# Optimization experiments

Measured on AMD Instinct MI355X. Metric: run time of the kernel, lower is better.

Reference implementation:

```python
import jax, jax.numpy as jnp
import numpy as np

N_NODES = 20000
N_EDGES = 320000
F_IN = 256
N_HID = 128
MID = 800


def _glorot(key, shape):
    fan_in, fan_out = shape
    s = jnp.sqrt(6.0 / (fan_in + fan_out))
    return jax.random.uniform(key, shape, jnp.float32, -s, s)


def setup_inputs() -> dict:
    key = jax.random.key(0)
    ks = jax.random.split(key, 8)
    x = jax.random.normal(ks[0], (N_NODES, F_IN), jnp.float32)
    src = jax.random.randint(ks[1], (N_EDGES,), 0, N_NODES)
    dst = jax.random.randint(ks[2], (N_EDGES,), 0, N_NODES)
    return {
        "x": x, "src": src, "dst": dst,
        "W1": _glorot(ks[3], (F_IN, MID)), "b1": jnp.zeros((MID,), jnp.float32),
        "W2": _glorot(ks[4], (MID, N_HID)), "b2": jnp.zeros((N_HID,), jnp.float32),
        "W3": _glorot(ks[5], (N_HID, MID)), "b3": jnp.zeros((MID,), jnp.float32),
        "W4": _glorot(ks[6], (MID, F_IN)), "b4": jnp.zeros((F_IN,), jnp.float32),
    }


def _deg_rsqrt(idx, n):
    # clamp(min=1) as in DGL GraphConv norm='both'
    deg = jax.ops.segment_sum(jnp.ones(idx.shape[0], jnp.float32), idx, num_segments=n)
    return jax.lax.rsqrt(jnp.maximum(deg, 1.0))


def _graph_conv(x, W, b, src, dst, n, act):
    # DGL GraphConv, norm='both': out = D_in^{-1/2} A D_out^{-1/2} X W + b
    ns = _deg_rsqrt(src, n)  # src-side (out-degree) norm
    nd = _deg_rsqrt(dst, n)  # dst-side (in-degree) norm
    in_f, out_f = W.shape
    if in_f > out_f:
        # multiply by W first (smaller aggregation width), as DGL does
        h = (x @ W) * ns[:, None]
        h = jax.ops.segment_sum(h[src], dst, num_segments=n)
    else:
        h = x * ns[:, None]
        h = jax.ops.segment_sum(h[src], dst, num_segments=n) @ W
    h = h * nd[:, None] + b
    return act(h) if act is not None else h


def reference(x, src, dst, W1, b1, W2, b2, W3, b3, W4, b4):
    n = x.shape[0]
    h = _graph_conv(x, W1, b1, src, dst, n, jax.nn.relu)   # [N, 800]
    h = _graph_conv(h, W2, b2, src, dst, n, None)          # [N, 128]
    encoded = jax.nn.sigmoid(h)
    h = _graph_conv(h, W3, b3, src, dst, n, jax.nn.relu)   # [N, 800]
    h = _graph_conv(h, W4, b4, src, dst, n, None)          # [N, 256]
    decoded = jax.nn.sigmoid(h)
    return (encoded, decoded)
```

## Files before the change

### kernel.cpp

```cpp
#include <hip/hip_runtime.h>
#include <math.h>

constexpr int NN = 20000;
constexpr int NE = 320000;
constexpr int MROWS = 20224;
constexpr int SB = 79;

typedef __bf16 bf16x8 __attribute__((ext_vector_type(8)));
typedef float f32x4 __attribute__((ext_vector_type(4)));

__device__ __forceinline__ unsigned short f2bf(float f) {
  unsigned int u = __float_as_uint(f);
  unsigned int r = (u + 0x7FFFu + ((u >> 16) & 1u)) >> 16;
  return (unsigned short)r;
}

__global__ __launch_bounds__(256) void zero_kernel(int4* __restrict__ p, int n4) {
  int i = blockIdx.x * 256 + threadIdx.x;
  if (i < n4) p[i] = make_int4(0, 0, 0, 0);
}

__global__ void deg_count_kernel(const int* __restrict__ src, const int* __restrict__ dst,
                                 int* __restrict__ degs, int* __restrict__ degd, int nE) {
  int e = blockIdx.x * blockDim.x + threadIdx.x;
  if (e < nE) {
    atomicAdd(degs + src[e], 1);
    atomicAdd(degd + dst[e], 1);
  }
}

__global__ __launch_bounds__(256) void pscan_norm_kernel(
    const int* __restrict__ degs, const int* __restrict__ degd,
    int* __restrict__ pscan, int* __restrict__ bsum,
    float* __restrict__ ns, float* __restrict__ nd, int n) {
  __shared__ int s[256];
  int t = threadIdx.x;
  int idx = blockIdx.x * 256 + t;
  int val = 0;
  if (idx < n) {
    int dd = degd[idx];
    val = dd;
    ns[idx] = rsqrtf(fmaxf((float)degs[idx], 1.0f));
    nd[idx] = rsqrtf(fmaxf((float)dd, 1.0f));
  }
  s[t] = val;
  __syncthreads();
#pragma unroll
  for (int off = 1; off < 256; off <<= 1) {
    int v = (t >= off) ? s[t - off] : 0;
    __syncthreads();
    s[t] += v;
    __syncthreads();
  }
  if (idx < n) pscan[idx] = s[t] - val;
  if (t == 255) bsum[blockIdx.x] = s[255];
}

__global__ __launch_bounds__(256) void rowptr_fix_kernel(
    const int* __restrict__ pscan, const int* __restrict__ bsum,
    int* __restrict__ rowptr, int n) {
  __shared__ int s[128];
  int t = threadIdx.x;
  if (t < 128) s[t] = (t < SB) ? bsum[t] : 0;
  __syncthreads();
#pragma unroll
  for (int off = 1; off < 128; off <<= 1) {
    int v = (t < 128 && t >= off) ? s[t - off] : 0;
    __syncthreads();
    if (t < 128) s[t] += v;
    __syncthreads();
  }
  int idx = blockIdx.x * 256 + t;
  int boff = (blockIdx.x == 0) ? 0 : s[blockIdx.x - 1];
  if (idx < n) rowptr[idx] = pscan[idx] + boff;
  if (idx == 0) rowptr[n] = NE;
}

__global__ void csr_fill_kernel(const int* __restrict__ src, const int* __restrict__ dst,
                                const int* __restrict__ rowptr, int* __restrict__ cursor,
                                int* __restrict__ col, int nE) {
  int e = blockIdx.x * blockDim.x + threadIdx.x;
  if (e < nE) {
    int d = dst[e];
    int p = atomicAdd(cursor + d, 1);
    col[rowptr[d] + p] = src[e];
  }
}

__global__ __launch_bounds__(256) void wt_convert_all_kernel(
    const float* __restrict__ W1, const float* __restrict__ W2,
    const float* __restrict__ W3, const float* __restrict__ W4,
    unsigned short* __restrict__ W1t, unsigned short* __restrict__ W2t,
    unsigned short* __restrict__ W3t, unsigned short* __restrict__ W4t) {
  int n = blockIdx.y;
  int k = blockIdx.x * 256 + threadIdx.x;
  const float* W; unsigned short* Wt; int K, N, Kpad;
  if (n < 832)       { W = W1; Wt = W1t; K = 256; N = 800; Kpad = 256; }
  else if (n < 960)  { n -= 832;  W = W2; Wt = W2t; K = 800; N = 128; Kpad = 832; }
  else if (n < 1792) { n -= 960;  W = W3; Wt = W3t; K = 128; N = 800; Kpad = 128; }
  else               { n -= 1792; W = W4; Wt = W4t; K = 800; N = 256; Kpad = 832; }
  if (k >= Kpad) return;
  float v = (n < N && k < K) ? W[(size_t)k * N + n] : 0.f;
  Wt[(size_t)n * Kpad + k] = f2bf(v);
}

__global__ __launch_bounds__(256) void scale_cvt_kernel(
    const float* __restrict__ x, const float* __restrict__ ns,
    unsigned short* __restrict__ xb) {
  int t = blockIdx.x * 256 + threadIdx.x;
  if (t >= NN * 32) return;
  int node = t >> 5;
  float sc = ns[node];
  float4 v1 = reinterpret_cast<const float4*>(x)[t * 2];
  float4 v2 = reinterpret_cast<const float4*>(x)[t * 2 + 1];
  uint4 o;
  o.x = f2bf(v1.x * sc) | ((unsigned)f2bf(v1.y * sc) << 16);
  o.y = f2bf(v1.z * sc) | ((unsigned)f2bf(v1.w * sc) << 16);
  o.z = f2bf(v2.x * sc) | ((unsigned)f2bf(v2.y * sc) << 16);
  o.w = f2bf(v2.z * sc) | ((unsigned)f2bf(v2.w * sc) << 16);
  reinterpret_cast<uint4*>(xb)[t] = o;
}

template <int F, int EPI>
__global__ __launch_bounds__(256) void gatherb_kernel(
    const unsigned short* __restrict__ in, const int* __restrict__ rowptr,
    const int* __restrict__ col, const float* __restrict__ sDst,
    const float* __restrict__ bias, const float* __restrict__ snext,
    unsigned short* __restrict__ out, float* __restrict__ out2, int n) {
  constexpr int LPN = F / 8;
  constexpr int NPB = 256 / LPN;
  const int tid = threadIdx.x;
  const int node = blockIdx.x * NPB + tid / LPN;
  const int j = tid % LPN;
  if (node >= n) return;
  const int e0 = rowptr[node], e1 = rowptr[node + 1];
  float a[8] = {0.f, 0.f, 0.f, 0.f, 0.f, 0.f, 0.f, 0.f};
  int e = e0;
  for (; e + 1 < e1; e += 2) {
    int c0 = col[e], c1 = col[e + 1];
    uint4 u0 = *reinterpret_cast<const uint4*>(in + (size_t)c0 * F + j * 8);
    uint4 u1 = *reinterpret_cast<const uint4*>(in + (size_t)c1 * F + j * 8);
    a[0] += __uint_as_float(u0.x << 16);
    a[1] += __uint_as_float(u0.x & 0xffff0000u);
    a[2] += __uint_as_float(u0.y << 16);
    a[3] += __uint_as_float(u0.y & 0xffff0000u);
    a[4] += __uint_as_float(u0.z << 16);
    a[5] += __uint_as_float(u0.z & 0xffff0000u);
    a[6] += __uint_as_float(u0.w << 16);
    a[7] += __uint_as_float(u0.w & 0xffff0000u);
    a[0] += __uint_as_float(u1.x << 16);
    a[1] += __uint_as_float(u1.x & 0xffff0000u);
    a[2] += __uint_as_float(u1.y << 16);
    a[3] += __uint_as_float(u1.y & 0xffff0000u);
    a[4] += __uint_as_float(u1.z << 16);
    a[5] += __uint_as_float(u1.z & 0xffff0000u);
    a[6] += __uint_as_float(u1.w << 16);
    a[7] += __uint_as_float(u1.w & 0xffff0000u);
  }
  if (e < e1) {
    int c = col[e];
    uint4 u = *reinterpret_cast<const uint4*>(in + (size_t)c * F + j * 8);
    a[0] += __uint_as_float(u.x << 16);
    a[1] += __uint_as_float(u.x & 0xffff0000u);
    a[2] += __uint_as_float(u.y << 16);
    a[3] += __uint_as_float(u.y & 0xffff0000u);
    a[4] += __uint_as_float(u.z << 16);
    a[5] += __uint_as_float(u.z & 0xffff0000u);
    a[6] += __uint_as_float(u.w << 16);
    a[7] += __uint_as_float(u.w & 0xffff0000u);
  }
  if (EPI == 0) {
    uint4 o;
    o.x = f2bf(a[0]) | ((unsigned)f2bf(a[1]) << 16);
    o.y = f2bf(a[2]) | ((unsigned)f2bf(a[3]) << 16);
    o.z = f2bf(a[4]) | ((unsigned)f2bf(a[5]) << 16);
    o.w = f2bf(a[6]) | ((unsigned)f2bf(a[7]) << 16);
    *reinterpret_cast<uint4*>(out + (size_t)node * F + j * 8) = o;
    return;
  }
  const float sd = sDst[node];
  float v[8];
#pragma unroll
  for (int k = 0; k < 8; ++k) v[k] = a[k] * sd + bias[j * 8 + k];
  if (EPI == 1) {
    float sn = snext[node];
    uint4 o;
    o.x = f2bf(v[0] * sn) | ((unsigned)f2bf(v[1] * sn) << 16);
    o.y = f2bf(v[2] * sn) | ((unsigned)f2bf(v[3] * sn) << 16);
    o.z = f2bf(v[4] * sn) | ((unsigned)f2bf(v[5] * sn) << 16);
    o.w = f2bf(v[6] * sn) | ((unsigned)f2bf(v[7] * sn) << 16);
    *reinterpret_cast<uint4*>(out + (size_t)node * F + j * 8) = o;
  }
  float4 s1, s2;
  s1.x = 1.0f / (1.0f + expf(-v[0]));
  s1.y = 1.0f / (1.0f + expf(-v[1]));
  s1.z = 1.0f / (1.0f + expf(-v[2]));
  s1.w = 1.0f / (1.0f + expf(-v[3]));
  s2.x = 1.0f / (1.0f + expf(-v[4]));
  s2.y = 1.0f / (1.0f + expf(-v[5]));
  s2.z = 1.0f / (1.0f + expf(-v[6]));
  s2.w = 1.0f / (1.0f + expf(-v[7]));
  *reinterpret_cast<float4*>(out2 + (size_t)node * F + j * 8) = s1;
  *reinterpret_cast<float4*>(out2 + (size_t)node * F + j * 8 + 4) = s2;
}

template <int KT1, int NOUT>
__global__ __launch_bounds__(256) void gemm9v2_kernel(
    const unsigned short* __restrict__ A,
    const unsigned short* __restrict__ Wa,
    const unsigned short* __restrict__ Wb,
    unsigned short* __restrict__ Out,
    int M, const float* __restrict__ nd, const float* __restrict__ ns,
    const float* __restrict__ ba) {
  constexpr int K1 = KT1 * 32;
  constexpr int N2 = NOUT * 16;
  constexpr int ROWB1 = K1 * 2;
  constexpr int CPR1 = K1 / 8;
  constexpr int W1B = 64 * ROWB1;
  constexpr int W2B = N2 * 128;
  constexpr int HST = 144;
  __shared__ __align__(16) char lds[W1B + W2B + 4 * 16 * HST];

  const int tid = threadIdx.x;
  const int l = tid & 63, w = tid >> 6;
  const int lrow = l & 15, k16 = l >> 4;
  const int m0 = blockIdx.x * 64 + w * 16;
  char* const w1p = lds;
  char* const w2s = lds + W1B;
  char* const h1t = lds + W1B + W2B + w * 16 * HST;

  auto stage = [&](int nt) {
#pragma unroll
    for (int i = 0; i < 64 * CPR1 / 256; ++i) {
      int c = i * 256 + tid;
      int row = c / CPR1, lch = c % CPR1;
      int gch = (lch & ~7) | ((lch & 7) ^ (row & 7));
      const unsigned short* gp = Wa + (size_t)(nt * 64 + row) * K1 + gch * 8;
      __builtin_amdgcn_global_load_lds(
          (const __attribute__((address_space(1))) void*)gp,
          (__attribute__((address_space(3))) void*)(w1p + (i * 256 + w * 64) * 16), 16, 0, 0);
    }
#pragma unroll
    for (int i = 0; i < N2 * 8 / 256; ++i) {
      int c = i * 256 + tid;
      int row = c >> 3, lch = c & 7;
      int gch = lch ^ (row & 7);
      const unsigned short* gp = Wb + (size_t)row * 832 + nt * 64 + gch * 8;
      __builtin_amdgcn_global_load_lds(
          (const __attribute__((address_space(1))) void*)gp,
          (__attribute__((address_space(3))) void*)(w2s + (i * 256 + w * 64) * 16), 16, 0, 0);
    }
  };

  bf16x8 af[KT1];
#pragma unroll
  for (int t = 0; t < KT1; ++t)
    af[t] = *reinterpret_cast<const bf16x8*>(
        A + (size_t)(m0 + lrow) * K1 + t * 32 + k16 * 8);

  stage(0);
  __syncthreads();

  f32x4 acc2[NOUT] = {};
  for (int nt = 0; nt < 13; ++nt) {
    f32x4 acc1[4] = {};
#pragma unroll
    for (int t = 0; t < KT1; ++t) {
      bf16x8 bf[4];
#pragma unroll
      for (int ni = 0; ni < 4; ++ni) {
        int row = ni * 16 + lrow;
        int ch = t * 4 + k16;
        int sc = (ch & ~7) | ((ch & 7) ^ (row & 7));
        bf[ni] = *reinterpret_cast<const bf16x8*>(w1p + row * ROWB1 + sc * 16);
      }
#pragma unroll
      for (int ni = 0; ni < 4; ++ni)
        acc1[ni] = __builtin_amdgcn_mfma_f32_16x16x32_bf16(af[t], bf[ni], acc1[ni], 0, 0, 0);
    }

#pragma unroll
    for (int q = 0; q < 4; ++q) {
      int rl = k16 * 4 + q;
      float rs = nd[m0 + rl];
#pragma unroll
      for (int ni = 0; ni < 4; ++ni) {
        int colc = ni * 16 + lrow;
        int jg = nt * 64 + colc;
        float bb = (jg < 800) ? ba[jg] : 0.f;
        float v = fmaxf(acc1[ni][q] * rs + bb, 0.f);
        *(unsigned short*)(h1t + rl * HST + (colc >> 3) * 16 + (colc & 7) * 2) = f2bf(v);
      }
    }

#pragma unroll
    for (int ks = 0; ks < 2; ++ks) {
      bf16x8 a2 = *reinterpret_cast<const bf16x8*>(h1t + lrow * HST + (ks * 4 + k16) * 16);
#pragma unroll
      for (int ni = 0; ni < NOUT; ++ni) {
        int rc = ni * 16 + lrow;
        int sc = (ks * 4 + k16) ^ (rc & 7);
        bf16x8 b2v = *reinterpret_cast<const bf16x8*>(w2s + rc * 128 + sc * 16);
        acc2[ni] = __builtin_amdgcn_mfma_f32_16x16x32_bf16(a2, b2v, acc2[ni], 0, 0, 0);
      }
    }
    __syncthreads();
    if (nt + 1 < 13) {
      stage(nt + 1);
      __syncthreads();
    }
  }

#pragma unroll
  for (int q = 0; q < 4; ++q) {
    int r = m0 + k16 * 4 + q;
    if (r >= M) continue;
    float sn = ns[r];
#pragma unroll
    for (int ni = 0; ni < NOUT; ++ni) {
      int c = ni * 16 + lrow;
      Out[(size_t)r * N2 + c] = f2bf(acc2[ni][q] * sn);
    }
  }
}

extern "C" void kernel_launch(void* const* d_in, const int* in_sizes, int n_in,
                              void* d_out, int out_size, void* d_ws, size_t ws_size,
                              hipStream_t stream) {
  const float* x  = (const float*)d_in[0];
  const int* src  = (const int*)d_in[1];
  const int* dst  = (const int*)d_in[2];
  const float* W1 = (const float*)d_in[3];
  const float* b1 = (const float*)d_in[4];
  const float* W2 = (const float*)d_in[5];
  const float* b2 = (const float*)d_in[6];
  const float* W3 = (const float*)d_in[7];
  const float* b3 = (const float*)d_in[8];
  const float* W4 = (const float*)d_in[9];
  const float* b4 = (const float*)d_in[10];

  float* out_enc = (float*)d_out;
  float* out_dec = out_enc + (size_t)NN * 128;

  float* ns = (float*)d_ws;
  float* nd = ns + NN;
  unsigned short* xb  = (unsigned short*)(nd + NN);
  unsigned short* T2b = xb + (size_t)NN * 256;
  unsigned short* h2  = T2b + (size_t)NN * 128;
  unsigned short* A1  = h2 + (size_t)NN * 128;
  unsigned short* A3  = A1 + (size_t)MROWS * 256;
  unsigned short* G4  = A3 + (size_t)MROWS * 128;
  unsigned short* W1t = G4 + (size_t)NN * 256;
  unsigned short* W2t = W1t + 832 * 256;
  unsigned short* W3t = W2t + 128 * 832;
  unsigned short* W4t = W3t + 832 * 128;
  int* degs   = (int*)(W4t + 256 * 832);
  int* degd   = degs + NN;
  int* cursor = degd + NN;
  int* rowptr = cursor + NN;
  int* col    = rowptr + NN + 1;
  int* pscan  = col + NE;
  int* bsum   = pscan + NN;

  zero_kernel<<<(3 * NN / 4 + 255) / 256, 256, 0, stream>>>((int4*)degs, 3 * NN / 4);
  deg_count_kernel<<<(NE + 255) / 256, 256, 0, stream>>>(src, dst, degs, degd, NE);
  pscan_norm_kernel<<<SB, 256, 0, stream>>>(degs, degd, pscan, bsum, ns, nd, NN);
  rowptr_fix_kernel<<<SB, 256, 0, stream>>>(pscan, bsum, rowptr, NN);
  csr_fill_kernel<<<(NE + 255) / 256, 256, 0, stream>>>(src, dst, rowptr, cursor, col, NE);

  wt_convert_all_kernel<<<dim3(4, 2048), 256, 0, stream>>>(
      W1, W2, W3, W4, W1t, W2t, W3t, W4t);

  scale_cvt_kernel<<<(NN * 32 + 255) / 256, 256, 0, stream>>>(x, ns, xb);
  gatherb_kernel<256, 0><<<(NN + 7) / 8, 256, 0, stream>>>(
      xb, rowptr, col, nullptr, nullptr, nullptr, A1, nullptr, NN);
  gemm9v2_kernel<8, 8><<<314, 256, 0, stream>>>(A1, W1t, W2t, T2b, NN, nd, ns, b1);

  gatherb_kernel<128, 1><<<(NN + 15) / 16, 256, 0, stream>>>(
      T2b, rowptr, col, nd, b2, ns, h2, out_enc, NN);

  gatherb_kernel<128, 0><<<(NN + 15) / 16, 256, 0, stream>>>(
      h2, rowptr, col, nullptr, nullptr, nullptr, A3, nullptr, NN);
  gemm9v2_kernel<4, 16><<<314, 256, 0, stream>>>(A3, W3t, W4t, G4, NN, nd, ns, b3);

  gatherb_kernel<256, 2><<<(NN + 7) / 8, 256, 0, stream>>>(
      G4, rowptr, col, nd, b4, nullptr, nullptr, out_dec, NN);
}
```

Before: 245.0 us.

## Split fused GEMM N-tiles across wave halves and read weights directly from global

The fused two-layer GEMM kernel no longer stages weight tiles into LDS with per-tile barriers. Instead each wave loads weight fragments straight from global memory, relying on L2/cache reuse. Each block now covers 32 rows, with the 13 middle-dimension tiles split between two wave pairs (7 and 6 tiles). The partial second-layer accumulators are reduced through LDS, and the launch grid doubles to 628 blocks. This removes the per-iteration __syncthreads and the LDS staging, and adds parallelism. The cost is more global/L2 weight traffic, uncoalesced-ish fragment loads, and a slightly unbalanced split.

```diff
diff --git a/kernel.cpp b/kernel.cpp
--- a/kernel.cpp
+++ b/kernel.cpp
@@ -205,7 +205,7 @@
 }
 
 template <int KT1, int NOUT>
-__global__ __launch_bounds__(256) void gemm9v2_kernel(
+__global__ __launch_bounds__(256) void gemm10_kernel(
     const unsigned short* __restrict__ A,
     const unsigned short* __restrict__ Wa,
     const unsigned short* __restrict__ Wb,
@@ -214,43 +214,19 @@
     const float* __restrict__ ba) {
   constexpr int K1 = KT1 * 32;
   constexpr int N2 = NOUT * 16;
-  constexpr int ROWB1 = K1 * 2;
-  constexpr int CPR1 = K1 / 8;
-  constexpr int W1B = 64 * ROWB1;
-  constexpr int W2B = N2 * 128;
   constexpr int HST = 144;
-  __shared__ __align__(16) char lds[W1B + W2B + 4 * 16 * HST];
+  constexpr int CST = N2 * 4 + 16;
+  constexpr int HTB = 4 * 16 * HST;
+  constexpr int CMB = 32 * CST;
+  constexpr int LDSB = (CMB > HTB ? CMB : HTB);
+  __shared__ __align__(16) char lds[LDSB];
 
   const int tid = threadIdx.x;
   const int l = tid & 63, w = tid >> 6;
+  const int wr = w & 1, half = w >> 1;
   const int lrow = l & 15, k16 = l >> 4;
-  const int m0 = blockIdx.x * 64 + w * 16;
-  char* const w1p = lds;
-  char* const w2s = lds + W1B;
-  char* const h1t = lds + W1B + W2B + w * 16 * HST;
-
-  auto stage = [&](int nt) {
-#pragma unroll
-    for (int i = 0; i < 64 * CPR1 / 256; ++i) {
-      int c = i * 256 + tid;
-      int row = c / CPR1, lch = c % CPR1;
-      int gch = (lch & ~7) | ((lch & 7) ^ (row & 7));
-      const unsigned short* gp = Wa + (size_t)(nt * 64 + row) * K1 + gch * 8;
-      __builtin_amdgcn_global_load_lds(
-          (const __attribute__((address_space(1))) void*)gp,
-          (__attribute__((address_space(3))) void*)(w1p + (i * 256 + w * 64) * 16), 16, 0, 0);
-    }
-#pragma unroll
-    for (int i = 0; i < N2 * 8 / 256; ++i) {
-      int c = i * 256 + tid;
-      int row = c >> 3, lch = c & 7;
-      int gch = lch ^ (row & 7);
-      const unsigned short* gp = Wb + (size_t)row * 832 + nt * 64 + gch * 8;
-      __builtin_amdgcn_global_load_lds(
-          (const __attribute__((address_space(1))) void*)gp,
-          (__attribute__((address_space(3))) void*)(w2s + (i * 256 + w * 64) * 16), 16, 0, 0);
-    }
-  };
+  const int m0 = blockIdx.x * 32 + wr * 16;
+  char* const h1t = lds + w * 16 * HST;
 
   bf16x8 af[KT1];
 #pragma unroll
@@ -258,22 +234,17 @@
     af[t] = *reinterpret_cast<const bf16x8*>(
         A + (size_t)(m0 + lrow) * K1 + t * 32 + k16 * 8);
 
-  stage(0);
-  __syncthreads();
-
   f32x4 acc2[NOUT] = {};
-  for (int nt = 0; nt < 13; ++nt) {
+  const int ntEnd = half ? 13 : 7;
+  for (int nt = half ? 7 : 0; nt < ntEnd; ++nt) {
     f32x4 acc1[4] = {};
 #pragma unroll
     for (int t = 0; t < KT1; ++t) {
       bf16x8 bf[4];
 #pragma unroll
-      for (int ni = 0; ni < 4; ++ni) {
-        int row = ni * 16 + lrow;
-        int ch = t * 4 + k16;
-        int sc = (ch & ~7) | ((ch & 7) ^ (row & 7));
-        bf[ni] = *reinterpret_cast<const bf16x8*>(w1p + row * ROWB1 + sc * 16);
-      }
+      for (int ni = 0; ni < 4; ++ni)
+        bf[ni] = *reinterpret_cast<const bf16x8*>(
+            Wa + (size_t)(nt * 64 + ni * 16 + lrow) * K1 + t * 32 + k16 * 8);
 #pragma unroll
       for (int ni = 0; ni < 4; ++ni)
         acc1[ni] = __builtin_amdgcn_mfma_f32_16x16x32_bf16(af[t], bf[ni], acc1[ni], 0, 0, 0);
@@ -298,28 +269,39 @@
       bf16x8 a2 = *reinterpret_cast<const bf16x8*>(h1t + lrow * HST + (ks * 4 + k16) * 16);
 #pragma unroll
       for (int ni = 0; ni < NOUT; ++ni) {
-        int rc = ni * 16 + lrow;
-        int sc = (ks * 4 + k16) ^ (rc & 7);
-        bf16x8 b2v = *reinterpret_cast<const bf16x8*>(w2s + rc * 128 + sc * 16);
+        bf16x8 b2v = *reinterpret_cast<const bf16x8*>(
+            Wb + (size_t)(ni * 16 + lrow) * 832 + nt * 64 + (ks * 4 + k16) * 8);
         acc2[ni] = __builtin_amdgcn_mfma_f32_16x16x32_bf16(a2, b2v, acc2[ni], 0, 0, 0);
       }
     }
-    __syncthreads();
-    if (nt + 1 < 13) {
-      stage(nt + 1);
-      __syncthreads();
-    }
-  }
-
-#pragma unroll
-  for (int q = 0; q < 4; ++q) {
-    int r = m0 + k16 * 4 + q;
-    if (r >= M) continue;
-    float sn = ns[r];
-#pragma unroll
-    for (int ni = 0; ni < NOUT; ++ni) {
-      int c = ni * 16 + lrow;
-      Out[(size_t)r * N2 + c] = f2bf(acc2[ni][q] * sn);
+  }
+
+  __syncthreads();
+  if (half) {
+#pragma unroll
+    for (int q = 0; q < 4; ++q) {
+      int rl = wr * 16 + k16 * 4 + q;
+#pragma unroll
+      for (int ni = 0; ni < NOUT; ++ni) {
+        int c = ni * 16 + lrow;
+        *(float*)(lds + rl * CST + c * 4) = acc2[ni][q];
+      }
+    }
+  }
+  __syncthreads();
+  if (!half) {
+#pragma unroll
+    for (int q = 0; q < 4; ++q) {
+      int r = m0 + k16 * 4 + q;
+      if (r >= M) continue;
+      int rl = wr * 16 + k16 * 4 + q;
+      float sn = ns[r];
+#pragma unroll
+      for (int ni = 0; ni < NOUT; ++ni) {
+        int c = ni * 16 + lrow;
+        float v = acc2[ni][q] + *(const float*)(lds + rl * CST + c * 4);
+        Out[(size_t)r * N2 + c] = f2bf(v * sn);
+      }
     }
   }
 }
@@ -374,14 +356,14 @@
   scale_cvt_kernel<<<(NN * 32 + 255) / 256, 256, 0, stream>>>(x, ns, xb);
   gatherb_kernel<256, 0><<<(NN + 7) / 8, 256, 0, stream>>>(
       xb, rowptr, col, nullptr, nullptr, nullptr, A1, nullptr, NN);
-  gemm9v2_kernel<8, 8><<<314, 256, 0, stream>>>(A1, W1t, W2t, T2b, NN, nd, ns, b1);
+  gemm10_kernel<8, 8><<<628, 256, 0, stream>>>(A1, W1t, W2t, T2b, NN, nd, ns, b1);
 
   gatherb_kernel<128, 1><<<(NN + 15) / 16, 256, 0, stream>>>(
       T2b, rowptr, col, nd, b2, ns, h2, out_enc, NN);
 
   gatherb_kernel<128, 0><<<(NN + 15) / 16, 256, 0, stream>>>(
       h2, rowptr, col, nullptr, nullptr, nullptr, A3, nullptr, NN);
-  gemm9v2_kernel<4, 16><<<314, 256, 0, stream>>>(A3, W3t, W4t, G4, NN, nd, ns, b3);
+  gemm10_kernel<4, 16><<<628, 256, 0, stream>>>(A3, W3t, W4t, G4, NN, nd, ns, b3);
 
   gatherb_kernel<256, 2><<<(NN + 7) / 8, 256, 0, stream>>>(
       G4, rowptr, col, nd, b4, nullptr, nullptr, out_dec, NN);
```

Result: slower. 421.4 us (+72.0%).

## Split fused GEMM hidden dimension across two wave halves with 32-row tiles

Applied to the files above, without the earlier changes.

The fused two-GEMM kernel now runs 512 threads per block on 128 rows. Each wave handles 32 rows, so every LDS weight fragment feeds two MFMAs. The two halves of the block split the 13 hidden-dimension tiles (7 and 6) and each stages its own weight buffers. Their partial second-GEMM accumulators are combined through LDS at the end. This roughly halves weight staging per row and the serial tile loop length, at the cost of more registers, more LDS, an extra reduction pass and half as many blocks.

```diff
diff --git a/kernel.cpp b/kernel.cpp
--- a/kernel.cpp
+++ b/kernel.cpp
@@ -205,7 +205,7 @@
 }
 
 template <int KT1, int NOUT>
-__global__ __launch_bounds__(256) void gemm9v2_kernel(
+__global__ __launch_bounds__(512) void gemm11_kernel(
     const unsigned short* __restrict__ A,
     const unsigned short* __restrict__ Wa,
     const unsigned short* __restrict__ Wb,
@@ -216,110 +216,151 @@
   constexpr int N2 = NOUT * 16;
   constexpr int ROWB1 = K1 * 2;
   constexpr int CPR1 = K1 / 8;
-  constexpr int W1B = 64 * ROWB1;
-  constexpr int W2B = N2 * 128;
+  constexpr int WaB = 64 * ROWB1;
+  constexpr int WbB = N2 * 128;
   constexpr int HST = 144;
-  __shared__ __align__(16) char lds[W1B + W2B + 4 * 16 * HST];
+  constexpr int CST = N2 * 4 + 16;
+  constexpr int STAGEB = 2 * WaB + 2 * WbB + 8 * 32 * HST;
+  constexpr int COMBB = 128 * CST;
+  constexpr int LDSB = (STAGEB > COMBB ? STAGEB : COMBB);
+  __shared__ __align__(16) char lds[LDSB];
 
   const int tid = threadIdx.x;
   const int l = tid & 63, w = tid >> 6;
+  const int g = w & 3, hh = w >> 2;
+  const int ht = tid & 255;
   const int lrow = l & 15, k16 = l >> 4;
-  const int m0 = blockIdx.x * 64 + w * 16;
-  char* const w1p = lds;
-  char* const w2s = lds + W1B;
-  char* const h1t = lds + W1B + W2B + w * 16 * HST;
+  const int m0 = blockIdx.x * 128 + g * 32;
+  char* const wa_h = lds + hh * WaB;
+  char* const wb_h = lds + 2 * WaB + hh * WbB;
+  char* const h1t = lds + 2 * WaB + 2 * WbB + w * 32 * HST;
 
   auto stage = [&](int nt) {
 #pragma unroll
     for (int i = 0; i < 64 * CPR1 / 256; ++i) {
-      int c = i * 256 + tid;
+      int c = i * 256 + ht;
       int row = c / CPR1, lch = c % CPR1;
       int gch = (lch & ~7) | ((lch & 7) ^ (row & 7));
       const unsigned short* gp = Wa + (size_t)(nt * 64 + row) * K1 + gch * 8;
       __builtin_amdgcn_global_load_lds(
           (const __attribute__((address_space(1))) void*)gp,
-          (__attribute__((address_space(3))) void*)(w1p + (i * 256 + w * 64) * 16), 16, 0, 0);
+          (__attribute__((address_space(3))) void*)(wa_h + (i * 256 + g * 64) * 16), 16, 0, 0);
     }
 #pragma unroll
     for (int i = 0; i < N2 * 8 / 256; ++i) {
-      int c = i * 256 + tid;
+      int c = i * 256 + ht;
       int row = c >> 3, lch = c & 7;
       int gch = lch ^ (row & 7);
       const unsigned short* gp = Wb + (size_t)row * 832 + nt * 64 + gch * 8;
       __builtin_amdgcn_global_load_lds(
           (const __attribute__((address_space(1))) void*)gp,
-          (__attribute__((address_space(3))) void*)(w2s + (i * 256 + w * 64) * 16), 16, 0, 0);
+          (__attribute__((address_space(3))) void*)(wb_h + (i * 256 + g * 64) * 16), 16, 0, 0);
     }
   };
 
-  bf16x8 af[KT1];
+  bf16x8 af[KT1][2];
 #pragma unroll
   for (int t = 0; t < KT1; ++t)
-    af[t] = *reinterpret_cast<const bf16x8*>(
-        A + (size_t)(m0 + lrow) * K1 + t * 32 + k16 * 8);
-
-  stage(0);
-  __syncthreads();
-
-  f32x4 acc2[NOUT] = {};
-  for (int nt = 0; nt < 13; ++nt) {
-    f32x4 acc1[4] = {};
-#pragma unroll
-    for (int t = 0; t < KT1; ++t) {
-      bf16x8 bf[4];
-#pragma unroll
-      for (int ni = 0; ni < 4; ++ni) {
-        int row = ni * 16 + lrow;
-        int ch = t * 4 + k16;
-        int sc = (ch & ~7) | ((ch & 7) ^ (row & 7));
-        bf[ni] = *reinterpret_cast<const bf16x8*>(w1p + row * ROWB1 + sc * 16);
+#pragma unroll
+    for (int mi = 0; mi < 2; ++mi)
+      af[t][mi] = *reinterpret_cast<const bf16x8*>(
+          A + (size_t)(m0 + mi * 16 + lrow) * K1 + t * 32 + k16 * 8);
+
+  f32x4 acc2[2][NOUT] = {};
+  for (int p = 0; p < 7; ++p) {
+    const bool act = (hh == 0) || (p < 6);
+    const int nt = hh ? 7 + p : p;
+    if (act) stage(nt);
+    __syncthreads();
+
+    if (act) {
+      f32x4 acc1[2][4] = {};
+#pragma unroll
+      for (int t = 0; t < KT1; ++t) {
+        bf16x8 bf[4];
+#pragma unroll
+        for (int ni = 0; ni < 4; ++ni) {
+          int row = ni * 16 + lrow;
+          int ch = t * 4 + k16;
+          int sc = (ch & ~7) | ((ch & 7) ^ (row & 7));
+          bf[ni] = *reinterpret_cast<const bf16x8*>(wa_h + row * ROWB1 + sc * 16);
+        }
+#pragma unroll
+        for (int mi = 0; mi < 2; ++mi)
+#pragma unroll
+          for (int ni = 0; ni < 4; ++ni)
+            acc1[mi][ni] = __builtin_amdgcn_mfma_f32_16x16x32_bf16(af[t][mi], bf[ni], acc1[mi][ni], 0, 0, 0);
       }
-#pragma unroll
-      for (int ni = 0; ni < 4; ++ni)
-        acc1[ni] = __builtin_amdgcn_mfma_f32_16x16x32_bf16(af[t], bf[ni], acc1[ni], 0, 0, 0);
-    }
-
-#pragma unroll
-    for (int q = 0; q < 4; ++q) {
-      int rl = k16 * 4 + q;
-      float rs = nd[m0 + rl];
-#pragma unroll
-      for (int ni = 0; ni < 4; ++ni) {
-        int colc = ni * 16 + lrow;
-        int jg = nt * 64 + colc;
-        float bb = (jg < 800) ? ba[jg] : 0.f;
-        float v = fmaxf(acc1[ni][q] * rs + bb, 0.f);
-        *(unsigned short*)(h1t + rl * HST + (colc >> 3) * 16 + (colc & 7) * 2) = f2bf(v);
+
+#pragma unroll
+      for (int mi = 0; mi < 2; ++mi) {
+#pragma unroll
+        for (int q = 0; q < 4; ++q) {
+          int rl = mi * 16 + k16 * 4 + q;
+          float rs = nd[m0 + rl];
+#pragma unroll
+          for (int ni = 0; ni < 4; ++ni) {
+            int colc = ni * 16 + lrow;
+            int jg = nt * 64 + colc;
+            float bb = (jg < 800) ? ba[jg] : 0.f;
+            float v = fmaxf(acc1[mi][ni][q] * rs + bb, 0.f);
+            *(unsigned short*)(h1t + rl * HST + (colc >> 3) * 16 + (colc & 7) * 2) = f2bf(v);
+          }
+        }
+      }
+
+#pragma unroll
+      for (int ks = 0; ks < 2; ++ks) {
+        bf16x8 a2[2];
+#pragma unroll
+        for (int mi = 0; mi < 2; ++mi)
+          a2[mi] = *reinterpret_cast<const bf16x8*>(
+              h1t + (mi * 16 + lrow) * HST + (ks * 4 + k16) * 16);
+#pragma unroll
+        for (int ni = 0; ni < NOUT; ++ni) {
+          int rc = ni * 16 + lrow;
+          int sc = (ks * 4 + k16) ^ (rc & 7);
+          bf16x8 b2v = *reinterpret_cast<const bf16x8*>(wb_h + rc * 128 + sc * 16);
+#pragma unroll
+          for (int mi = 0; mi < 2; ++mi)
+            acc2[mi][ni] = __builtin_amdgcn_mfma_f32_16x16x32_bf16(a2[mi], b2v, acc2[mi][ni], 0, 0, 0);
+        }
       }
     }
-
-#pragma unroll
-    for (int ks = 0; ks < 2; ++ks) {
-      bf16x8 a2 = *reinterpret_cast<const bf16x8*>(h1t + lrow * HST + (ks * 4 + k16) * 16);
-#pragma unroll
-      for (int ni = 0; ni < NOUT; ++ni) {
-        int rc = ni * 16 + lrow;
-        int sc = (ks * 4 + k16) ^ (rc & 7);
-        bf16x8 b2v = *reinterpret_cast<const bf16x8*>(w2s + rc * 128 + sc * 16);
-        acc2[ni] = __builtin_amdgcn_mfma_f32_16x16x32_bf16(a2, b2v, acc2[ni], 0, 0, 0);
+    __syncthreads();
+  }
+
+  if (hh == 1) {
+#pragma unroll
+    for (int mi = 0; mi < 2; ++mi) {
+#pragma unroll
+      for (int q = 0; q < 4; ++q) {
+        int rb = g * 32 + mi * 16 + k16 * 4 + q;
+#pragma unroll
+        for (int ni = 0; ni < NOUT; ++ni) {
+          int c = ni * 16 + lrow;
+          *(float*)(lds + rb * CST + c * 4) = acc2[mi][ni][q];
+        }
       }
     }
-    __syncthreads();
-    if (nt + 1 < 13) {
-      stage(nt + 1);
-      __syncthreads();
-    }
-  }
-
-#pragma unroll
-  for (int q = 0; q < 4; ++q) {
-    int r = m0 + k16 * 4 + q;
-    if (r >= M) continue;
-    float sn = ns[r];
-#pragma unroll
-    for (int ni = 0; ni < NOUT; ++ni) {
-      int c = ni * 16 + lrow;
-      Out[(size_t)r * N2 + c] = f2bf(acc2[ni][q] * sn);
+  }
+  __syncthreads();
+  if (hh == 0) {
+#pragma unroll
+    for (int mi = 0; mi < 2; ++mi) {
+#pragma unroll
+      for (int q = 0; q < 4; ++q) {
+        int r = m0 + mi * 16 + k16 * 4 + q;
+        if (r >= M) continue;
+        int rb = g * 32 + mi * 16 + k16 * 4 + q;
+        float sn = ns[r];
+#pragma unroll
+        for (int ni = 0; ni < NOUT; ++ni) {
+          int c = ni * 16 + lrow;
+          float v = acc2[mi][ni][q] + *(const float*)(lds + rb * CST + c * 4);
+          Out[(size_t)r * N2 + c] = f2bf(v * sn);
+        }
+      }
     }
   }
 }
@@ -374,14 +415,14 @@
   scale_cvt_kernel<<<(NN * 32 + 255) / 256, 256, 0, stream>>>(x, ns, xb);
   gatherb_kernel<256, 0><<<(NN + 7) / 8, 256, 0, stream>>>(
       xb, rowptr, col, nullptr, nullptr, nullptr, A1, nullptr, NN);
-  gemm9v2_kernel<8, 8><<<314, 256, 0, stream>>>(A1, W1t, W2t, T2b, NN, nd, ns, b1);
+  gemm11_kernel<8, 8><<<157, 512, 0, stream>>>(A1, W1t, W2t, T2b, NN, nd, ns, b1);
 
   gatherb_kernel<128, 1><<<(NN + 15) / 16, 256, 0, stream>>>(
       T2b, rowptr, col, nd, b2, ns, h2, out_enc, NN);
 
   gatherb_kernel<128, 0><<<(NN + 15) / 16, 256, 0, stream>>>(
       h2, rowptr, col, nullptr, nullptr, nullptr, A3, nullptr, NN);
-  gemm9v2_kernel<4, 16><<<314, 256, 0, stream>>>(A3, W3t, W4t, G4, NN, nd, ns, b3);
+  gemm11_kernel<4, 16><<<157, 512, 0, stream>>>(A3, W3t, W4t, G4, NN, nd, ns, b3);
 
   gatherb_kernel<256, 2><<<(NN + 7) / 8, 256, 0, stream>>>(
       G4, rowptr, col, nd, b4, nullptr, nullptr, out_dec, NN);
```

Measured after the change: 280.6 us. +14.5%, slower.
